# Kernel tuning notes

Measured on AMD Instinct MI355X. Metric: run time of the kernel, lower is better.

The kernel has to match this reference:

```python
import jax, jax.numpy as jnp
import numpy as np

B, L, N, C = 64, 12, 4096, 3
FD, HD, OUT = 32, 64, 12
TID, DIW, TD = 288, 7, 16
STEPS = 4
EMB = 10  # node embedding dim for learned adjacency


def setup_inputs() -> dict:
    key = jax.random.key(0)
    ks = jax.random.split(key, 16)
    g = lambda i, shape, s=0.05: jax.random.normal(ks[i], shape, dtype=jnp.float32) * s
    z = lambda n: jnp.zeros((n,), jnp.float32)
    return {
        "history_data": jax.random.uniform(ks[0], (B, L, N, C), dtype=jnp.float32),
        "future_data": jnp.zeros((B, L, N, 1), jnp.float32),
        "batch_seen": 0,
        "epoch": 0,
        "train": 1,
        "tid_emb": g(1, (TID, TD)),
        "diw_emb": g(2, (DIW, TD)),
        "t2f_w": g(3, (2 * TD, FD)), "t2f_b": z(FD),
        "enc_w1": g(4, (L * C, HD)), "enc_b1": z(HD),
        "enc_w2": g(5, (HD, FD)), "enc_b2": z(FD),
        "node_emb": g(6, (N, EMB), 1.0),
        "pde_w1": g(7, (FD, HD)), "pde_b1": z(HD),
        "pde_w2": g(8, (HD, FD)), "pde_b2": z(FD),
        "ss_win": g(9, (FD, FD)), "ss_wst": g(10, (FD, FD)), "ss_b": z(FD),
        "ss_wout": g(11, (FD, FD)), "ss_bout": z(FD),
        "dec_w1": g(12, (FD, HD)), "dec_b1": z(HD),
        "dec_w2": g(13, (HD, OUT)), "dec_b2": z(OUT),
        "pde_mix": jnp.array(0.5, jnp.float32),
    }


def reference(history_data, future_data, batch_seen, epoch, train,
              tid_emb, diw_emb, t2f_w, t2f_b,
              enc_w1, enc_b1, enc_w2, enc_b2,
              node_emb,
              pde_w1, pde_b1, pde_w2, pde_b2,
              ss_win, ss_wst, ss_b, ss_wout, ss_bout,
              dec_w1, dec_b1, dec_w2, dec_b2, pde_mix):
    # --- encoder: per-node MLP over flattened (L, C) history ---
    x = history_data[..., :C]                                    # [B,L,N,C]
    x = jnp.transpose(x, (0, 2, 1, 3)).reshape(B, N, L * C)      # [B,N,L*C]
    field = jnp.maximum(x @ enc_w1 + enc_b1, 0.0) @ enc_w2 + enc_b2  # [B,N,FD]

    # --- temporal field bias from last-step tid/diw ---
    tid_idx = jnp.clip((history_data[:, -1, :, 1] * TID).astype(jnp.int32), 0, TID - 1)
    diw_idx = jnp.clip((history_data[:, -1, :, 2] * DIW).astype(jnp.int32), 0, DIW - 1)
    temp = jnp.concatenate([tid_emb[tid_idx], diw_emb[diw_idx]], axis=-1)  # [B,N,2*TD]
    field = field + temp @ t2f_w + t2f_b

    # --- learned adjacency for graph Laplacian (L = I - A) ---
    A = jax.nn.softmax(jnp.maximum(node_emb @ node_emb.T, 0.0), axis=-1)  # [N,N]

    alpha = jax.nn.sigmoid(pde_mix)
    dt = 1.0 / STEPS
    state = jnp.zeros_like(field)
    for _ in range(STEPS):  # fixed small unroll over PDE steps
        L_F = jnp.einsum('nm,bmf->bnf', A, field) - field         # (A - I) F
        N_F = jnp.maximum(field @ pde_w1 + pde_b1, 0.0) @ pde_w2 + pde_b2
        fe = field + (alpha * L_F + (1.0 - alpha) * N_F) * dt
        state = jnp.tanh(fe @ ss_win + state @ ss_wst + ss_b)     # state-space update
        field = fe + state @ ss_wout + ss_bout

    # --- decoder: per-node MLP to output horizon ---
    pred = jnp.maximum(field @ dec_w1 + dec_b1, 0.0) @ dec_w2 + dec_b2  # [B,N,OUT]
    return jnp.transpose(pred, (0, 2, 1))[..., None]              # [B,OUT,N,1]
```

## Files before the change

kernel.cpp:

```cpp
#include <hip/hip_runtime.h>

#define BATCH 64
#define LHIST 12
#define NNODE 4096
#define CCH   3
#define FD    32
#define HD    64
#define OUTD  12
#define TIDN  288
#define DIWN  7
#define TDD   16
#define EMBD  10
#define MROWS 2048
#define KDIM  4096
#define MTOT  (BATCH * NNODE)

typedef __attribute__((ext_vector_type(8))) short bf16x8;
typedef __attribute__((ext_vector_type(4))) float f32x4;

union BF8U { bf16x8 v; unsigned short s[8]; };

__device__ __forceinline__ unsigned short f2b(float f) {
    union { float f; unsigned u; } v; v.f = f;
    unsigned r = v.u + 0x7fffu + ((v.u >> 16) & 1u);
    return (unsigned short)(r >> 16);
}

__device__ __forceinline__ float fast_tanh(float x) {
    x = fminf(fmaxf(x, -15.f), 15.f);
    const float e = __expf(2.f * x);
    return (e - 1.f) / (e + 1.f);
}

__device__ __forceinline__ void gl2lds16(const void* g, void* l) {
    __builtin_amdgcn_global_load_lds((__attribute__((address_space(1))) void*)(void*)g,
                                     (__attribute__((address_space(3))) void*)l, 16, 0, 0);
}

__device__ __forceinline__ bf16x8 ldsfrag(const unsigned short* p) {
    return *(const bf16x8*)p;
}

__device__ __forceinline__ bf16x8 pack8(float4 a, float4 b) {
    BF8U u;
    u.s[0] = f2b(a.x); u.s[1] = f2b(a.y); u.s[2] = f2b(a.z); u.s[3] = f2b(a.w);
    u.s[4] = f2b(b.x); u.s[5] = f2b(b.y); u.s[6] = f2b(b.z); u.s[7] = f2b(b.w);
    return u.v;
}

__global__ __launch_bounds__(256) void build_A(const float* __restrict__ emb,
                                               unsigned short* __restrict__ A) {
    const int n = blockIdx.x;
    const int tid = threadIdx.x;
    __shared__ float sc[NNODE];
    __shared__ float red[256];
    float e[EMBD];
#pragma unroll
    for (int c = 0; c < EMBD; c++) e[c] = emb[(size_t)n * EMBD + c];
    float mx = 0.f;
    for (int m = tid; m < NNODE; m += 256) {
        float s = 0.f;
#pragma unroll
        for (int c = 0; c < EMBD; c++) s += e[c] * emb[(size_t)m * EMBD + c];
        s = fmaxf(s, 0.f);
        sc[m] = s;
        mx = fmaxf(mx, s);
    }
    red[tid] = mx;
    __syncthreads();
    for (int off = 128; off > 0; off >>= 1) {
        if (tid < off) red[tid] = fmaxf(red[tid], red[tid + off]);
        __syncthreads();
    }
    mx = red[0];
    __syncthreads();
    float sum = 0.f;
    for (int m = tid; m < NNODE; m += 256) {
        float v = expf(sc[m] - mx);
        sc[m] = v;
        sum += v;
    }
    red[tid] = sum;
    __syncthreads();
    for (int off = 128; off > 0; off >>= 1) {
        if (tid < off) red[tid] += red[tid + off];
        __syncthreads();
    }
    const float inv = 1.f / red[0];
    for (int m = tid; m < NNODE; m += 256)
        A[(size_t)n * NNODE + m] = f2b(sc[m] * inv);
}

__global__ __launch_bounds__(256, 2) void encoder(const float* __restrict__ hist,
                                                  const float* __restrict__ tid_emb,
                                                  const float* __restrict__ diw_emb,
                                                  const float* __restrict__ t2f_w,
                                                  const float* __restrict__ t2f_b,
                                                  const float* __restrict__ enc_w1,
                                                  const float* __restrict__ enc_b1,
                                                  const float* __restrict__ enc_w2,
                                                  const float* __restrict__ enc_b2,
                                                  float* __restrict__ field,
                                                  unsigned short* __restrict__ fT) {
    const int gid = blockIdx.x * 256 + threadIdx.x;
    const int b = gid >> 12;
    const int n = gid & (NNODE - 1);
    const float* hb = hist + ((size_t)b * LHIST * NNODE + n) * CCH;
    float x[LHIST * CCH];
#pragma unroll
    for (int l = 0; l < LHIST; l++) {
        x[l * 3 + 0] = hb[(size_t)l * NNODE * CCH + 0];
        x[l * 3 + 1] = hb[(size_t)l * NNODE * CCH + 1];
        x[l * 3 + 2] = hb[(size_t)l * NNODE * CCH + 2];
    }
    float f[FD];
#pragma unroll
    for (int o = 0; o < FD; o++) f[o] = enc_b2[o] + t2f_b[o];
    for (int j = 0; j < HD; j++) {
        float h = enc_b1[j];
#pragma unroll
        for (int k = 0; k < LHIST * CCH; k++) h += x[k] * enc_w1[k * HD + j];
        h = fmaxf(h, 0.f);
#pragma unroll
        for (int o = 0; o < FD; o++) f[o] += h * enc_w2[j * FD + o];
    }
    const int ti = min(max((int)(x[11 * 3 + 1] * 288.0f), 0), TIDN - 1);
    const int di = min(max((int)(x[11 * 3 + 2] * 7.0f), 0), DIWN - 1);
    for (int g = 0; g < TDD; g++) {
        const float tg = tid_emb[ti * TDD + g];
        const float dg = diw_emb[di * TDD + g];
#pragma unroll
        for (int o = 0; o < FD; o++)
            f[o] += tg * t2f_w[g * FD + o] + dg * t2f_w[(TDD + g) * FD + o];
    }
#pragma unroll
    for (int o4 = 0; o4 < FD / 4; o4++) {
        float4 v = {f[o4 * 4 + 0], f[o4 * 4 + 1], f[o4 * 4 + 2], f[o4 * 4 + 3]};
        *(float4*)&field[(size_t)gid * FD + o4 * 4] = v;
    }
#pragma unroll
    for (int o = 0; o < FD; o++)
        fT[(size_t)(b * FD + o) * NNODE + n] = f2b(f[o]);
}

__global__ __launch_bounds__(256) void gemm_bt(const unsigned short* __restrict__ X,
                                               const unsigned short* __restrict__ Y,
                                               float* __restrict__ C) {
    constexpr int K = KDIM;
    constexpr int BK = 32;
    __shared__ __align__(16) unsigned short Xs[128 * BK];
    __shared__ __align__(16) unsigned short Ys[128 * BK];
    const int tid = threadIdx.x;
    const int wave = tid >> 6;
    const int lane = tid & 63;
    const int i0 = blockIdx.x * 128;
    const int j0 = blockIdx.y * 128;
    const int wi = (wave >> 1) * 64;
    const int wj = (wave & 1) * 64;

    const int lrow = lane >> 2;
    const int lcol = (lane & 3) * 8;

    const unsigned short* Xg = X + (size_t)(i0 + wave * 32 + lrow) * K + lcol;
    const unsigned short* Yg = Y + (size_t)(j0 + wave * 32 + lrow) * K + lcol;
    unsigned short* Xl0 = &Xs[(wave * 32) * BK];
    unsigned short* Xl1 = &Xs[(wave * 32 + 16) * BK];
    unsigned short* Yl0 = &Ys[(wave * 32) * BK];
    unsigned short* Yl1 = &Ys[(wave * 32 + 16) * BK];

    const f32x4 zero = {0.f, 0.f, 0.f, 0.f};
    f32x4 acc[4][4];
#pragma unroll
    for (int a = 0; a < 4; a++)
#pragma unroll
        for (int b = 0; b < 4; b++) acc[a][b] = zero;

    const int fr = lane & 15;
    const int kq = (lane >> 4) * 8;

    for (int kt = 0; kt < K; kt += BK) {
        __syncthreads();
        gl2lds16(Xg + kt, Xl0);
        gl2lds16(Xg + kt + 16 * K, Xl1);
        gl2lds16(Yg + kt, Yl0);
        gl2lds16(Yg + kt + 16 * K, Yl1);
        __syncthreads();
        bf16x8 fa[4], fb[4];
#pragma unroll
        for (int t = 0; t < 4; t++)
            fa[t] = *(const bf16x8*)&Xs[(wi + t * 16 + fr) * BK + kq];
#pragma unroll
        for (int t = 0; t < 4; t++)
            fb[t] = *(const bf16x8*)&Ys[(wj + t * 16 + fr) * BK + kq];
#pragma unroll
        for (int mi = 0; mi < 4; mi++)
#pragma unroll
            for (int ni = 0; ni < 4; ni++)
                acc[mi][ni] = __builtin_amdgcn_mfma_f32_16x16x32_bf16(
                    fa[mi], fb[ni], acc[mi][ni], 0, 0, 0);
    }

    const int r0 = (lane >> 4) * 4;
#pragma unroll
    for (int mi = 0; mi < 4; mi++) {
#pragma unroll
        for (int ni = 0; ni < 4; ni++) {
            const int R0 = i0 + wi + mi * 16 + r0;
            const int col = j0 + wj + ni * 16 + fr;
            const size_t addr = ((size_t)(R0 >> 5) * NNODE + col) * FD + (R0 & 31);
            *(f32x4*)&C[addr] = acc[mi][ni];
        }
    }
}

#define HPAD 72
#define FPAD 40
__global__ __launch_bounds__(256, 2) void step_mfma(const float* __restrict__ Ct,
                                                    float* __restrict__ field,
                                                    float* __restrict__ state,
                                                    unsigned short* __restrict__ fT,
                                                    const float* __restrict__ pde_w1,
                                                    const float* __restrict__ pde_b1,
                                                    const float* __restrict__ pde_w2,
                                                    const float* __restrict__ pde_b2,
                                                    const float* __restrict__ ss_win,
                                                    const float* __restrict__ ss_wst,
                                                    const float* __restrict__ ss_b,
                                                    const float* __restrict__ ss_wout,
                                                    const float* __restrict__ ss_bout,
                                                    const float* __restrict__ pde_mix,
                                                    int first) {
    __shared__ __align__(16) unsigned short W1T[HD * FD];
    __shared__ __align__(16) unsigned short W2T[FD * HD];
    __shared__ __align__(16) unsigned short WinT[FD * FD];
    __shared__ __align__(16) unsigned short WstT[FD * FD];
    __shared__ __align__(16) unsigned short WoutT[FD * FD];
    __shared__ __align__(16) unsigned short Hs[4 * 64 * HPAD];
    __shared__ __align__(16) unsigned short Fs[4 * 64 * FPAD];

    const int tid = threadIdx.x;
    for (int i = tid; i < HD * FD; i += 256) W1T[(i & 63) * FD + (i >> 6)] = f2b(pde_w1[i]);
    for (int i = tid; i < HD * FD; i += 256) W2T[(i & 31) * HD + (i >> 5)] = f2b(pde_w2[i]);
    for (int i = tid; i < FD * FD; i += 256) {
        WinT [(i & 31) * FD + (i >> 5)] = f2b(ss_win[i]);
        WstT [(i & 31) * FD + (i >> 5)] = f2b(ss_wst[i]);
        WoutT[(i & 31) * FD + (i >> 5)] = f2b(ss_wout[i]);
    }
    __syncthreads();

    const int wv = tid >> 6;
    const int lane = tid & 63;
    const int ln = lane & 15;
    const int q = lane >> 4;
    const int kq = q * 8;
    const int r0 = q * 4;
    const int mw = blockIdx.x * 256 + wv * 64;
    const int b = mw >> 12;
    const int n0 = mw & (NNODE - 1);
    unsigned short* Hw = &Hs[wv * 64 * HPAD];
    unsigned short* Fw = &Fs[wv * 64 * FPAD];

    const float alpha = 1.f / (1.f + __expf(-pde_mix[0]));
    const float dt = 0.25f;

    bf16x8 w1f[4], w2f[2][2], winf[2], wstf[2], woutf[2];
#pragma unroll
    for (int nj = 0; nj < 4; nj++) w1f[nj] = ldsfrag(&W1T[(nj * 16 + ln) * FD + kq]);
#pragma unroll
    for (int nf = 0; nf < 2; nf++) {
#pragma unroll
        for (int kk = 0; kk < 2; kk++)
            w2f[nf][kk] = ldsfrag(&W2T[(nf * 16 + ln) * HD + kk * 32 + kq]);
        winf[nf]  = ldsfrag(&WinT [(nf * 16 + ln) * FD + kq]);
        wstf[nf]  = ldsfrag(&WstT [(nf * 16 + ln) * FD + kq]);
        woutf[nf] = ldsfrag(&WoutT[(nf * 16 + ln) * FD + kq]);
    }

    float b1v[4], b2v[2], bsv[2], bov[2];
#pragma unroll
    for (int nj = 0; nj < 4; nj++) b1v[nj] = pde_b1[nj * 16 + ln];
#pragma unroll
    for (int nf = 0; nf < 2; nf++) {
        b2v[nf] = pde_b2[nf * 16 + ln];
        bsv[nf] = ss_b[nf * 16 + ln];
        bov[nf] = ss_bout[nf * 16 + ln];
    }

    bf16x8 fA[4], stA[4];
#pragma unroll
    for (int mi = 0; mi < 4; mi++) {
        const float4* fp = (const float4*)&field[(size_t)(mw + mi * 16 + ln) * FD + kq];
        fA[mi] = pack8(fp[0], fp[1]);
    }
    if (!first) {
#pragma unroll
        for (int mi = 0; mi < 4; mi++) {
            const float4* sp = (const float4*)&state[(size_t)(mw + mi * 16 + ln) * FD + kq];
            stA[mi] = pack8(sp[0], sp[1]);
        }
    }

    const f32x4 zero = {0.f, 0.f, 0.f, 0.f};

    f32x4 hc[4][4];
#pragma unroll
    for (int mi = 0; mi < 4; mi++)
#pragma unroll
        for (int nj = 0; nj < 4; nj++)
            hc[mi][nj] = __builtin_amdgcn_mfma_f32_16x16x32_bf16(fA[mi], w1f[nj], zero, 0, 0, 0);
#pragma unroll
    for (int mi = 0; mi < 4; mi++)
#pragma unroll
        for (int nj = 0; nj < 4; nj++)
#pragma unroll
            for (int r = 0; r < 4; r++)
                Hw[(mi * 16 + r0 + r) * HPAD + nj * 16 + ln] =
                    f2b(fmaxf(hc[mi][nj][r] + b1v[nj], 0.f));
    __syncthreads();

    float fld[4][2][4], ctv[4][2][4];
#pragma unroll
    for (int mi = 0; mi < 4; mi++)
#pragma unroll
        for (int nf = 0; nf < 2; nf++)
#pragma unroll
            for (int r = 0; r < 4; r++) {
                const size_t idx = (size_t)(mw + mi * 16 + r0 + r) * FD + nf * 16 + ln;
                fld[mi][nf][r] = field[idx];
                ctv[mi][nf][r] = Ct[idx];
            }

    bf16x8 hA[4][2];
#pragma unroll
    for (int mi = 0; mi < 4; mi++)
#pragma unroll
        for (int kk = 0; kk < 2; kk++)
            hA[mi][kk] = ldsfrag(&Hw[(mi * 16 + ln) * HPAD + kk * 32 + kq]);
    f32x4 nc[4][2];
#pragma unroll
    for (int mi = 0; mi < 4; mi++)
#pragma unroll
        for (int nf = 0; nf < 2; nf++) {
            f32x4 a = __builtin_amdgcn_mfma_f32_16x16x32_bf16(hA[mi][0], w2f[nf][0], zero, 0, 0, 0);
            nc[mi][nf] = __builtin_amdgcn_mfma_f32_16x16x32_bf16(hA[mi][1], w2f[nf][1], a, 0, 0, 0);
        }

    float fe[4][2][4];
#pragma unroll
    for (int mi = 0; mi < 4; mi++)
#pragma unroll
        for (int nf = 0; nf < 2; nf++)
#pragma unroll
            for (int r = 0; r < 4; r++) {
                const float nfv = nc[mi][nf][r] + b2v[nf];
                const float fv = fld[mi][nf][r];
                fe[mi][nf][r] = fv + (alpha * (ctv[mi][nf][r] - fv) + (1.f - alpha) * nfv) * dt;
                Fw[(mi * 16 + r0 + r) * FPAD + nf * 16 + ln] = f2b(fe[mi][nf][r]);
            }
    __syncthreads();

    bf16x8 feA[4];
#pragma unroll
    for (int mi = 0; mi < 4; mi++) feA[mi] = ldsfrag(&Fw[(mi * 16 + ln) * FPAD + kq]);
    f32x4 sc_[4][2];
#pragma unroll
    for (int mi = 0; mi < 4; mi++)
#pragma unroll
        for (int nf = 0; nf < 2; nf++) {
            f32x4 a = __builtin_amdgcn_mfma_f32_16x16x32_bf16(feA[mi], winf[nf], zero, 0, 0, 0);
            if (!first)
                a = __builtin_amdgcn_mfma_f32_16x16x32_bf16(stA[mi], wstf[nf], a, 0, 0, 0);
            sc_[mi][nf] = a;
        }
    float sval[4][2][4];
#pragma unroll
    for (int mi = 0; mi < 4; mi++)
#pragma unroll
        for (int nf = 0; nf < 2; nf++)
#pragma unroll
            for (int r = 0; r < 4; r++) {
                sval[mi][nf][r] = fast_tanh(sc_[mi][nf][r] + bsv[nf]);
            }
    __syncthreads();
#pragma unroll
    for (int mi = 0; mi < 4; mi++)
#pragma unroll
        for (int nf = 0; nf < 2; nf++)
#pragma unroll
            for (int r = 0; r < 4; r++)
                Fw[(mi * 16 + r0 + r) * FPAD + nf * 16 + ln] = f2b(sval[mi][nf][r]);
    __syncthreads();

    bf16x8 SA[4];
#pragma unroll
    for (int mi = 0; mi < 4; mi++) SA[mi] = ldsfrag(&Fw[(mi * 16 + ln) * FPAD + kq]);
#pragma unroll
    for (int mi = 0; mi < 4; mi++) {
#pragma unroll
        for (int nf = 0; nf < 2; nf++) {
            f32x4 oc = __builtin_amdgcn_mfma_f32_16x16x32_bf16(SA[mi], woutf[nf], zero, 0, 0, 0);
            float fnew[4];
#pragma unroll
            for (int r = 0; r < 4; r++) {
                fnew[r] = fe[mi][nf][r] + oc[r] + bov[nf];
                const size_t idx = (size_t)(mw + mi * 16 + r0 + r) * FD + nf * 16 + ln;
                field[idx] = fnew[r];
                state[idx] = sval[mi][nf][r];
            }
            ushort4 pk = {f2b(fnew[0]), f2b(fnew[1]), f2b(fnew[2]), f2b(fnew[3])};
            const size_t ft_addr = (size_t)(b * FD + nf * 16 + ln) * NNODE + n0 + mi * 16 + r0;
            *(ushort4*)&fT[ft_addr] = pk;
        }
    }
}

__global__ __launch_bounds__(256, 2) void decoder(const float* __restrict__ field,
                                                  const float* __restrict__ dw1,
                                                  const float* __restrict__ db1,
                                                  const float* __restrict__ dw2,
                                                  const float* __restrict__ db2,
                                                  float* __restrict__ out) {
    const int gid = blockIdx.x * 256 + threadIdx.x;
    const int b = gid >> 12;
    const int n = gid & (NNODE - 1);
    float ff[FD];
#pragma unroll
    for (int o4 = 0; o4 < FD / 4; o4++) {
        float4 v = *(const float4*)&field[(size_t)gid * FD + o4 * 4];
        ff[o4 * 4 + 0] = v.x; ff[o4 * 4 + 1] = v.y; ff[o4 * 4 + 2] = v.z; ff[o4 * 4 + 3] = v.w;
    }
    float o[OUTD];
#pragma unroll
    for (int t = 0; t < OUTD; t++) o[t] = db2[t];
    for (int j = 0; j < HD; j++) {
        float h = db1[j];
#pragma unroll
        for (int k = 0; k < FD; k++) h += ff[k] * dw1[k * HD + j];
        h = fmaxf(h, 0.f);
#pragma unroll
        for (int t = 0; t < OUTD; t++) o[t] += h * dw2[j * OUTD + t];
    }
#pragma unroll
    for (int t = 0; t < OUTD; t++)
        out[(size_t)(b * OUTD + t) * NNODE + n] = o[t];
}

extern "C" void kernel_launch(void* const* d_in, const int* in_sizes, int n_in,
                              void* d_out, int out_size, void* d_ws, size_t ws_size,
                              hipStream_t stream) {
    (void)in_sizes; (void)n_in; (void)out_size; (void)ws_size;
    const float* hist    = (const float*)d_in[0];
    const float* tid_emb = (const float*)d_in[5];
    const float* diw_emb = (const float*)d_in[6];
    const float* t2f_w   = (const float*)d_in[7];
    const float* t2f_b   = (const float*)d_in[8];
    const float* enc_w1  = (const float*)d_in[9];
    const float* enc_b1  = (const float*)d_in[10];
    const float* enc_w2  = (const float*)d_in[11];
    const float* enc_b2  = (const float*)d_in[12];
    const float* node_emb= (const float*)d_in[13];
    const float* pde_w1  = (const float*)d_in[14];
    const float* pde_b1  = (const float*)d_in[15];
    const float* pde_w2  = (const float*)d_in[16];
    const float* pde_b2  = (const float*)d_in[17];
    const float* ss_win  = (const float*)d_in[18];
    const float* ss_wst  = (const float*)d_in[19];
    const float* ss_b    = (const float*)d_in[20];
    const float* ss_wout = (const float*)d_in[21];
    const float* ss_bout = (const float*)d_in[22];
    const float* dec_w1  = (const float*)d_in[23];
    const float* dec_b1  = (const float*)d_in[24];
    const float* dec_w2  = (const float*)d_in[25];
    const float* dec_b2  = (const float*)d_in[26];
    const float* pde_mix = (const float*)d_in[27];

    char* w = (char*)d_ws;
    unsigned short* A_bf = (unsigned short*)w;  w += (size_t)KDIM * KDIM * 2;
    unsigned short* fT   = (unsigned short*)w;  w += (size_t)MROWS * KDIM * 2;
    float* field = (float*)w;                   w += (size_t)MTOT * FD * 4;
    float* state = (float*)w;                   w += (size_t)MTOT * FD * 4;
    float* Ct    = (float*)w;                   w += (size_t)MTOT * FD * 4;

    build_A<<<NNODE, 256, 0, stream>>>(node_emb, A_bf);
    encoder<<<(BATCH * NNODE) / 256, 256, 0, stream>>>(hist, tid_emb, diw_emb, t2f_w,
                                                       t2f_b, enc_w1, enc_b1, enc_w2,
                                                       enc_b2, field, fT);
    for (int s = 0; s < 4; s++) {
        gemm_bt<<<dim3(MROWS / 128, KDIM / 128), 256, 0, stream>>>(fT, A_bf, Ct);
        step_mfma<<<MTOT / 256, 256, 0, stream>>>(
            Ct, field, state, fT, pde_w1, pde_b1, pde_w2, pde_b2, ss_win, ss_wst,
            ss_b, ss_wout, ss_bout, pde_mix, s == 0 ? 1 : 0);
    }
    decoder<<<(BATCH * NNODE) / 256, 256, 0, stream>>>(field, dec_w1, dec_b1, dec_w2,
                                                       dec_b2, (float*)d_out);
}
```

Measured before the change: 819.8 us.

## Split-K graph GEMM with XCD-aware tile mapping, LDS swizzle, bf16 partials

The graph-propagation GEMM is split along K into two halves. This doubles the grid from 512 to 1024 blocks so more CUs are occupied, and the step kernel sums the two partial results. Block indices are remapped so that tiles sharing A columns land on the same XCD for L2 reuse, and an XOR swizzle is applied to the LDS layout to reduce bank conflicts. The partial outputs and the state buffer are stored in bf16 to halve their memory traffic, at the cost of extra rounding error in the Laplacian term and the recurrent state.

```diff
diff --git a/kernel.cpp b/kernel.cpp
--- a/kernel.cpp
+++ b/kernel.cpp
@@ -24,6 +24,10 @@
     union { float f; unsigned u; } v; v.f = f;
     unsigned r = v.u + 0x7fffu + ((v.u >> 16) & 1u);
     return (unsigned short)(r >> 16);
+}
+
+__device__ __forceinline__ float b2f(unsigned short u) {
+    union { unsigned u; float f; } v; v.u = (unsigned)u << 16; return v.f;
 }
 
 __device__ __forceinline__ float fast_tanh(float x) {
@@ -145,24 +149,34 @@
 
 __global__ __launch_bounds__(256) void gemm_bt(const unsigned short* __restrict__ X,
                                                const unsigned short* __restrict__ Y,
-                                               float* __restrict__ C) {
+                                               unsigned short* __restrict__ Cp) {
     constexpr int K = KDIM;
+    constexpr int KS = KDIM / 2;
     constexpr int BK = 32;
     __shared__ __align__(16) unsigned short Xs[128 * BK];
     __shared__ __align__(16) unsigned short Ys[128 * BK];
     const int tid = threadIdx.x;
     const int wave = tid >> 6;
     const int lane = tid & 63;
-    const int i0 = blockIdx.x * 128;
-    const int j0 = blockIdx.y * 128;
+
+    const int l = blockIdx.x + 16 * blockIdx.y;
+    const int xcd = l & 7;
+    const int rem = l >> 3;
+    const int by = xcd * 4 + (rem & 3);
+    const int bx = rem >> 2;
+    const int i0 = bx * 128;
+    const int j0 = by * 128;
+    const int k0 = blockIdx.z * KS;
+    unsigned short* C = Cp + (size_t)blockIdx.z * MTOT * FD;
+
     const int wi = (wave >> 1) * 64;
     const int wj = (wave & 1) * 64;
 
     const int lrow = lane >> 2;
-    const int lcol = (lane & 3) * 8;
-
-    const unsigned short* Xg = X + (size_t)(i0 + wave * 32 + lrow) * K + lcol;
-    const unsigned short* Yg = Y + (size_t)(j0 + wave * 32 + lrow) * K + lcol;
+    const int lcol = ((lane & 3) ^ ((lane >> 3) & 3)) * 8;
+
+    const unsigned short* Xg = X + (size_t)(i0 + wave * 32 + lrow) * K + k0 + lcol;
+    const unsigned short* Yg = Y + (size_t)(j0 + wave * 32 + lrow) * K + k0 + lcol;
     unsigned short* Xl0 = &Xs[(wave * 32) * BK];
     unsigned short* Xl1 = &Xs[(wave * 32 + 16) * BK];
     unsigned short* Yl0 = &Ys[(wave * 32) * BK];
@@ -176,9 +190,10 @@
         for (int b = 0; b < 4; b++) acc[a][b] = zero;
 
     const int fr = lane & 15;
-    const int kq = (lane >> 4) * 8;
-
-    for (int kt = 0; kt < K; kt += BK) {
+    const int q = lane >> 4;
+    const int kq = (q ^ ((fr >> 1) & 3)) * 8;
+
+    for (int kt = 0; kt < KS; kt += BK) {
         __syncthreads();
         gl2lds16(Xg + kt, Xl0);
         gl2lds16(Xg + kt + 16 * K, Xl1);
@@ -200,7 +215,7 @@
                     fa[mi], fb[ni], acc[mi][ni], 0, 0, 0);
     }
 
-    const int r0 = (lane >> 4) * 4;
+    const int r0 = q * 4;
 #pragma unroll
     for (int mi = 0; mi < 4; mi++) {
 #pragma unroll
@@ -208,16 +223,19 @@
             const int R0 = i0 + wi + mi * 16 + r0;
             const int col = j0 + wj + ni * 16 + fr;
             const size_t addr = ((size_t)(R0 >> 5) * NNODE + col) * FD + (R0 & 31);
-            *(f32x4*)&C[addr] = acc[mi][ni];
+            ushort4 pk = {f2b(acc[mi][ni][0]), f2b(acc[mi][ni][1]),
+                          f2b(acc[mi][ni][2]), f2b(acc[mi][ni][3])};
+            *(ushort4*)&C[addr] = pk;
         }
     }
 }
 
 #define HPAD 72
 #define FPAD 40
-__global__ __launch_bounds__(256, 2) void step_mfma(const float* __restrict__ Ct,
+__global__ __launch_bounds__(256, 2) void step_mfma(const unsigned short* __restrict__ Ct0,
+                                                    const unsigned short* __restrict__ Ct1,
                                                     float* __restrict__ field,
-                                                    float* __restrict__ state,
+                                                    unsigned short* __restrict__ state,
                                                     unsigned short* __restrict__ fT,
                                                     const float* __restrict__ pde_w1,
                                                     const float* __restrict__ pde_b1,
@@ -294,10 +312,8 @@
     }
     if (!first) {
 #pragma unroll
-        for (int mi = 0; mi < 4; mi++) {
-            const float4* sp = (const float4*)&state[(size_t)(mw + mi * 16 + ln) * FD + kq];
-            stA[mi] = pack8(sp[0], sp[1]);
-        }
+        for (int mi = 0; mi < 4; mi++)
+            stA[mi] = *(const bf16x8*)&state[(size_t)(mw + mi * 16 + ln) * FD + kq];
     }
 
     const f32x4 zero = {0.f, 0.f, 0.f, 0.f};
@@ -327,7 +343,7 @@
             for (int r = 0; r < 4; r++) {
                 const size_t idx = (size_t)(mw + mi * 16 + r0 + r) * FD + nf * 16 + ln;
                 fld[mi][nf][r] = field[idx];
-                ctv[mi][nf][r] = Ct[idx];
+                ctv[mi][nf][r] = b2f(Ct0[idx]) + b2f(Ct1[idx]);
             }
 
     bf16x8 hA[4][2];
@@ -378,9 +394,8 @@
 #pragma unroll
         for (int nf = 0; nf < 2; nf++)
 #pragma unroll
-            for (int r = 0; r < 4; r++) {
+            for (int r = 0; r < 4; r++)
                 sval[mi][nf][r] = fast_tanh(sc_[mi][nf][r] + bsv[nf]);
-            }
     __syncthreads();
 #pragma unroll
     for (int mi = 0; mi < 4; mi++)
@@ -405,7 +420,7 @@
                 fnew[r] = fe[mi][nf][r] + oc[r] + bov[nf];
                 const size_t idx = (size_t)(mw + mi * 16 + r0 + r) * FD + nf * 16 + ln;
                 field[idx] = fnew[r];
-                state[idx] = sval[mi][nf][r];
+                state[idx] = f2b(sval[mi][nf][r]);
             }
             ushort4 pk = {f2b(fnew[0]), f2b(fnew[1]), f2b(fnew[2]), f2b(fnew[3])};
             const size_t ft_addr = (size_t)(b * FD + nf * 16 + ln) * NNODE + n0 + mi * 16 + r0;
@@ -478,18 +493,18 @@
     unsigned short* A_bf = (unsigned short*)w;  w += (size_t)KDIM * KDIM * 2;
     unsigned short* fT   = (unsigned short*)w;  w += (size_t)MROWS * KDIM * 2;
     float* field = (float*)w;                   w += (size_t)MTOT * FD * 4;
-    float* state = (float*)w;                   w += (size_t)MTOT * FD * 4;
-    float* Ct    = (float*)w;                   w += (size_t)MTOT * FD * 4;
+    unsigned short* state = (unsigned short*)w; w += (size_t)MTOT * FD * 2;
+    unsigned short* Cp    = (unsigned short*)w; w += (size_t)2 * MTOT * FD * 2;
 
     build_A<<<NNODE, 256, 0, stream>>>(node_emb, A_bf);
     encoder<<<(BATCH * NNODE) / 256, 256, 0, stream>>>(hist, tid_emb, diw_emb, t2f_w,
                                                        t2f_b, enc_w1, enc_b1, enc_w2,
                                                        enc_b2, field, fT);
     for (int s = 0; s < 4; s++) {
-        gemm_bt<<<dim3(MROWS / 128, KDIM / 128), 256, 0, stream>>>(fT, A_bf, Ct);
+        gemm_bt<<<dim3(16, 32, 2), 256, 0, stream>>>(fT, A_bf, Cp);
         step_mfma<<<MTOT / 256, 256, 0, stream>>>(
-            Ct, field, state, fT, pde_w1, pde_b1, pde_w2, pde_b2, ss_win, ss_wst,
-            ss_b, ss_wout, ss_bout, pde_mix, s == 0 ? 1 : 0);
+            Cp, Cp + (size_t)MTOT * FD, field, state, fT, pde_w1, pde_b1, pde_w2,
+            pde_b2, ss_win, ss_wst, ss_b, ss_wout, ss_bout, pde_mix, s == 0 ? 1 : 0);
     }
     decoder<<<(BATCH * NNODE) / 256, 256, 0, stream>>>(field, dec_w1, dec_b1, dec_w2,
                                                        dec_b2, (float*)d_out);
```

Result: faster. 769.9 us (-6.1%).
